# Optimization experiments

Measured on AMD Instinct MI355X. Metric: run time of the kernel, lower is better.

Reference implementation:

```python
import jax, jax.numpy as jnp
import numpy as np

DIM = 256; NH = 8; WH = 8; WW = 8; N = WH * WW
B, T, M, H, W = 2, 4, 5, 64, 64
HD = DIM // NH
SCALE = HD ** -0.5

def _rel_pos_index():
    coords = np.stack(np.meshgrid(np.arange(WH), np.arange(WW), indexing='ij'))
    cf = coords.reshape(2, -1)
    rc = (cf[:, :, None] - cf[:, None, :]).transpose(1, 2, 0)
    rc[:, :, 0] += WH - 1
    rc[:, :, 1] += WW - 1
    rc[:, :, 0] *= 2 * WW - 1
    return rc.sum(-1)  # (N, N) ints in [0, (2WH-1)(2WW-1))

RPI = _rel_pos_index()

def layer_norm(x, g, b, eps=1e-5):
    mu = x.mean(-1, keepdims=True)
    var = jnp.mean((x - mu) ** 2, axis=-1, keepdims=True)
    return (x - mu) * jax.lax.rsqrt(var + eps) * g + b

def setup_inputs():
    key = jax.random.key(0)
    ks = jax.random.split(key, 32)
    C = DIM
    w = lambda i, shape, s=0.02: jax.random.normal(ks[i], shape, jnp.float32) * s
    return {
        'x': jax.random.normal(ks[0], (B, T, H, W, C), jnp.float32),
        'kv': jax.random.normal(ks[1], (B, M, H, W, C), jnp.float32),
        'mask_matrix': jnp.zeros(((H // WH) * (W // WW), N, N), jnp.float32),
        'norm_q_g': jnp.ones((C,), jnp.float32), 'norm_q_b': jnp.zeros((C,), jnp.float32),
        'norm_kv_g': jnp.ones((C,), jnp.float32), 'norm_kv_b': jnp.zeros((C,), jnp.float32),
        'q_w': w(2, (C, C)), 'q_b': w(3, (C,)),
        'kv_w': w(4, (2 * C, C)), 'kv_b': w(5, (2 * C,)),
        'rpb_table': w(6, ((2 * WH - 1) * (2 * WW - 1), NH)),
        'pos_emb': jax.random.normal(ks[7], (N, C), jnp.float32) / C ** 0.5,
        'pq_w': w(8, (C, C)), 'pq_b': w(9, (C,)),
        'pk_w': w(10, (C, C)), 'pk_b': w(11, (C,)),
        'pv_w': w(12, (C, C)), 'pv_b': w(13, (C,)),
        'po_w': w(14, (C, C)), 'po_b': w(15, (C,)),
        'proj_w': w(16, (C, C)), 'proj_b': w(17, (C,)),
        'norm2_g': jnp.ones((C,), jnp.float32), 'norm2_b': jnp.zeros((C,), jnp.float32),
        'mlp_w1': w(18, (4 * C, C)), 'mlp_b1': w(19, (4 * C,)),
        'mlp_w2': w(20, (C, 4 * C)), 'mlp_b2': w(21, (C,)),
    }

def _attention_pool(xw, pos_emb, pq_w, pq_b, pk_w, pk_b, pv_w, pv_b, po_w, po_b):
    # CLIP-style attention pooling: xw (b, M, N, C) -> (b, N, C)
    b, m, n, C = xw.shape
    avg = xw.mean(axis=1, keepdims=True)
    xw = jnp.concatenate([avg, xw], axis=1) + pos_emb[None, None]  # (b, M+1, N, C)
    tok = xw.reshape(b, (m + 1) * n, C)  # flattened (m n) token axis
    q = (tok[:, :n] @ pq_w.T + pq_b).reshape(b, n, NH, HD).transpose(0, 2, 1, 3) * HD ** -0.5
    k = (tok @ pk_w.T + pk_b).reshape(b, -1, NH, HD).transpose(0, 2, 1, 3)
    v = (tok @ pv_w.T + pv_b).reshape(b, -1, NH, HD).transpose(0, 2, 1, 3)
    a = jax.nn.softmax(jnp.einsum('bhqd,bhkd->bhqk', q, k), axis=-1)
    o = jnp.einsum('bhqk,bhkd->bhqd', a, v).transpose(0, 2, 1, 3).reshape(b, n, C)
    return o @ po_w.T + po_b

def reference(x, kv, mask_matrix, norm_q_g, norm_q_b, norm_kv_g, norm_kv_b,
              q_w, q_b, kv_w, kv_b, rpb_table, pos_emb,
              pq_w, pq_b, pk_w, pk_b, pv_w, pv_b, po_w, po_b,
              proj_w, proj_b, norm2_g, norm2_b, mlp_w1, mlp_b1, mlp_w2, mlp_b2):
    Bv, Tv, Hv, Wv, C = x.shape
    Mv = kv.shape[1]
    nWh, nWw = Hv // WH, Wv // WW
    nW = nWh * nWw
    B_ = Bv * nW
    shortcut = x
    xq = layer_norm(x, norm_q_g, norm_q_b)
    xk = layer_norm(kv, norm_kv_g, norm_kv_b)

    def part(z, S):  # window partition (B,S,H,W,C) -> (B*nW, S, N, C)
        z = z.reshape(Bv, S, nWh, WH, nWw, WW, C)
        return z.transpose(0, 2, 4, 1, 3, 5, 6).reshape(B_, S, N, C)

    qw = part(xq, Tv)
    kvw = part(xk, Mv)
    q = (qw @ q_w.T + q_b).reshape(B_, Tv, N, NH, HD).transpose(0, 1, 3, 2, 4)   # (B_,T,h,N,d)
    kvp = (kvw @ kv_w.T + kv_b).reshape(B_, Mv, N, 2, NH, HD)
    k = kvp[:, :, :, 0].transpose(0, 1, 3, 2, 4)                                  # (B_,M,h,N,d)
    v = kvp[:, :, :, 1].transpose(0, 1, 3, 2, 4)
    attn = jnp.einsum('bthnd,bmhkd->btmhnk', q * SCALE, k)                        # (B_,T,M,h,N,N)
    rpb = rpb_table[RPI.reshape(-1)].reshape(N, N, NH).transpose(2, 0, 1)         # (h,N,N)
    attn = jax.nn.softmax(attn + rpb[None, None, None], axis=-1)  # shift=(0,0) -> mask_matrix unused
    out = jnp.einsum('btmhnk,bmhkd->btmhnd', attn, v)                             # (B_,T,M,h,N,d)
    # faithful to torch: transpose(1,2) (swap T/M) then flat reshape to (B_,T,M,N,C)
    out = out.transpose(0, 2, 1, 3, 4, 5).reshape(B_, Tv, Mv, N, C)
    out = out.reshape(B_ * Tv, Mv, N, C)
    out = _attention_pool(out, pos_emb, pq_w, pq_b, pk_w, pk_b, pv_w, pv_b, po_w, po_b)
    out = out.reshape(B_, Tv, N, C)
    out = jax.nn.gelu(out, approximate=False)
    out = out @ proj_w.T + proj_b
    # window reverse -> (B,T,H,W,C)
    out = out.reshape(Bv, nWh, nWw, Tv, WH, WW, C).transpose(0, 3, 1, 4, 2, 5, 6).reshape(Bv, Tv, Hv, Wv, C)
    x1 = shortcut + out
    h = layer_norm(x1, norm2_g, norm2_b)
    h = jax.nn.gelu(h @ mlp_w1.T + mlp_b1, approximate=False) @ mlp_w2.T + mlp_b2
    return x1 + h
```

## Files before the change

kernel.cpp:

```cpp
#include <hip/hip_runtime.h>
#include <hip/hip_bf16.h>
#include <cstddef>
#include <cstdint>

#define SCALE_QK 0.17677669529663687f

typedef __attribute__((ext_vector_type(8))) short bf16x8;
typedef __attribute__((ext_vector_type(4))) float f32x4;

__global__ __launch_bounds__(256) void convb_kernel(
    const float* __restrict__ src, __hip_bfloat16* __restrict__ dst, int n) {
  int i = blockIdx.x * 256 + threadIdx.x;
  if (i < n) dst[i] = __float2bfloat16(src[i]);
}

__global__ __launch_bounds__(256) void rpbx_kernel(
    const float* __restrict__ rpb_table, ushort* __restrict__ rpbx) {
  int gid = blockIdx.x * 256 + threadIdx.x;
  int h = gid >> 12;
  int rest = gid & 4095;
  int n = rest >> 6, j = rest & 63;
  int i1 = n >> 3, j1 = n & 7, i2 = j >> 3, j2 = j & 7;
  float v = rpb_table[((i1 - i2 + 7) * 15 + (j1 - j2 + 7)) * 8 + h];
  __hip_bfloat16 b = __float2bfloat16(v);
  rpbx[gid] = *reinterpret_cast<ushort*>(&b);
}

__global__ __launch_bounds__(256) void ln_part_kernel(
    const float* __restrict__ in, __hip_bfloat16* __restrict__ out,
    const float* __restrict__ gamma, const float* __restrict__ beta,
    int S, int b0) {
  int r = blockIdx.x;
  int n = r & 63;
  int tmp = r >> 6;
  int s = tmp % S;
  int b_ = b0 + tmp / S;
  int b  = b_ >> 6;
  int wh = (b_ >> 3) & 7;
  int ww = b_ & 7;
  int gh = wh * 8 + (n >> 3);
  int gw = ww * 8 + (n & 7);
  const float* src = in + (((size_t)(b * S + s) * 64 + gh) * 64 + gw) * 256;
  int c = threadIdx.x;
  float v = src[c];
  __shared__ float red[256];
  red[c] = v; __syncthreads();
  for (int off = 128; off > 0; off >>= 1) { if (c < off) red[c] += red[c + off]; __syncthreads(); }
  float mu = red[0] * (1.f / 256.f);
  __syncthreads();
  float dv = v - mu;
  red[c] = dv * dv; __syncthreads();
  for (int off = 128; off > 0; off >>= 1) { if (c < off) red[c] += red[c + off]; __syncthreads(); }
  float var = red[0] * (1.f / 256.f);
  out[(size_t)r * 256 + c] = __float2bfloat16(dv * rsqrtf(var + 1e-5f) * gamma[c] + beta[c]);
}

__global__ __launch_bounds__(256) void ln_plain_kernel(
    const float* __restrict__ in, __hip_bfloat16* __restrict__ out,
    const float* __restrict__ gamma, const float* __restrict__ beta) {
  int r = blockIdx.x;
  const float* src = in + (size_t)r * 256;
  int c = threadIdx.x;
  float v = src[c];
  __shared__ float red[256];
  red[c] = v; __syncthreads();
  for (int off = 128; off > 0; off >>= 1) { if (c < off) red[c] += red[c + off]; __syncthreads(); }
  float mu = red[0] * (1.f / 256.f);
  __syncthreads();
  float dv = v - mu;
  red[c] = dv * dv; __syncthreads();
  for (int off = 128; off > 0; off >>= 1) { if (c < off) red[c] += red[c + off]; __syncthreads(); }
  float var = red[0] * (1.f / 256.f);
  out[(size_t)r * 256 + c] = __float2bfloat16(dv * rsqrtf(var + 1e-5f) * gamma[c] + beta[c]);
}

__global__ __launch_bounds__(256) void mgemm_kernel(
    const ushort* __restrict__ A, const ushort* __restrict__ W,
    const float* __restrict__ bias, const float* __restrict__ resid,
    void* __restrict__ Cp, int Mrows, int N, int K, int flags) {
  __shared__ ushort As[128 * 64];
  __shared__ ushort Bs[128 * 64];
  int tid = threadIdx.x;
  int lane = tid & 63, wid = tid >> 6;
  int wm = wid >> 1, wn = wid & 1;
  int row0 = blockIdx.y * 128, col0 = blockIdx.x * 128;
  int srow = tid >> 3;
  int slot = tid & 7;
  f32x4 acc[4][4];
  #pragma unroll
  for (int m = 0; m < 4; ++m)
    #pragma unroll
    for (int n = 0; n < 4; ++n) acc[m][n] = (f32x4){0.f, 0.f, 0.f, 0.f};

  for (int k0 = 0; k0 < K; k0 += 64) {
    #pragma unroll
    for (int i = 0; i < 4; ++i) {
      int r = i * 32 + srow;
      int gr = row0 + r; if (gr >= Mrows) gr = Mrows - 1;
      bf16x8 va = *(const bf16x8*)(A + (size_t)gr * K + k0 + slot * 8);
      int gc = col0 + r;
      bf16x8 vb = *(const bf16x8*)(W + (size_t)gc * K + k0 + slot * 8);
      int ldso = r * 64 + ((slot ^ (r & 7)) << 3);
      *(bf16x8*)(As + ldso) = va;
      *(bf16x8*)(Bs + ldso) = vb;
    }
    __syncthreads();
    #pragma unroll
    for (int ks = 0; ks < 2; ++ks) {
      bf16x8 af[4], bfr[4];
      int sgrp = ks * 4 + (lane >> 4);
      #pragma unroll
      for (int m = 0; m < 4; ++m) {
        int r = wm * 64 + m * 16 + (lane & 15);
        af[m] = *(const bf16x8*)(As + r * 64 + ((sgrp ^ (r & 7)) << 3));
      }
      #pragma unroll
      for (int n = 0; n < 4; ++n) {
        int r = wn * 64 + n * 16 + (lane & 15);
        bfr[n] = *(const bf16x8*)(Bs + r * 64 + ((sgrp ^ (r & 7)) << 3));
      }
      #pragma unroll
      for (int m = 0; m < 4; ++m)
        #pragma unroll
        for (int n = 0; n < 4; ++n)
          acc[m][n] = __builtin_amdgcn_mfma_f32_16x16x32_bf16(af[m], bfr[n], acc[m][n], 0, 0, 0);
    }
    __syncthreads();
  }

  float* Cf = (float*)Cp;
  __hip_bfloat16* Cb = (__hip_bfloat16*)Cp;
  #pragma unroll
  for (int m = 0; m < 4; ++m) {
    #pragma unroll
    for (int n = 0; n < 4; ++n) {
      int col = col0 + wn * 64 + n * 16 + (lane & 15);
      #pragma unroll
      for (int r = 0; r < 4; ++r) {
        int row = row0 + wm * 64 + m * 16 + (lane >> 4) * 4 + r;
        if (row >= Mrows) continue;
        float v = acc[m][n][r] + (bias ? bias[col] : 0.f);
        if (flags & 1) v = 0.5f * v * (1.f + erff(v * 0.70710678118654752f));
        if (resid) v += resid[(size_t)row * N + col];
        if (flags & 2) Cb[(size_t)row * N + col] = __float2bfloat16(v);
        else           Cf[(size_t)row * N + col] = v;
      }
    }
  }
}

#define TBM 64
#define TBN 64
#define TBK 16
__global__ __launch_bounds__(256) void gemm_kernel(
    const float* __restrict__ A, const float* __restrict__ Wt,
    const float* __restrict__ bias, float* __restrict__ Cc,
    int Mrows, int Nout, int K) {
  __shared__ float Asl[TBK][TBM + 1];
  __shared__ float Wsl[TBK][TBN + 1];
  int tid = threadIdx.x;
  int tx = tid & 15, ty = tid >> 4;
  int row0 = blockIdx.y * TBM, col0 = blockIdx.x * TBN;
  float acc[4][4] = {};
  for (int k0 = 0; k0 < K; k0 += TBK) {
    #pragma unroll
    for (int t = 0; t < 4; ++t) {
      int idx = t * 256 + tid;
      int lm = idx >> 4, lk = idx & 15;
      int gr = row0 + lm;
      Asl[lk][lm] = (gr < Mrows) ? A[(size_t)gr * K + k0 + lk] : 0.f;
      int gc = col0 + lm;
      Wsl[lk][lm] = (gc < Nout) ? Wt[(size_t)gc * K + k0 + lk] : 0.f;
    }
    __syncthreads();
    #pragma unroll
    for (int kk = 0; kk < TBK; ++kk) {
      float a[4], b[4];
      #pragma unroll
      for (int i = 0; i < 4; ++i) a[i] = Asl[kk][ty * 4 + i];
      #pragma unroll
      for (int j = 0; j < 4; ++j) b[j] = Wsl[kk][tx * 4 + j];
      #pragma unroll
      for (int i = 0; i < 4; ++i)
        #pragma unroll
        for (int j = 0; j < 4; ++j)
          acc[i][j] = fmaf(a[i], b[j], acc[i][j]);
    }
    __syncthreads();
  }
  #pragma unroll
  for (int i = 0; i < 4; ++i) {
    int gr = row0 + ty * 4 + i;
    if (gr >= Mrows) continue;
    #pragma unroll
    for (int j = 0; j < 4; ++j) {
      int gc = col0 + tx * 4 + j;
      if (gc >= Nout) continue;
      Cc[(size_t)gr * Nout + gc] = acc[i][j] + bias[gc];
    }
  }
}

__global__ __launch_bounds__(256) void wattn_kernel(
    const float* __restrict__ qb, const float* __restrict__ kvp,
    const ushort* __restrict__ rpbx, __hip_bfloat16* __restrict__ xw) {
  int idx = blockIdx.x;
  int h = idx & 7; idx >>= 3;
  int m = idx % 5;
  int b_l = idx / 5;
  int tid = threadIdx.x;
  int n = tid & 63;
  int w = tid >> 6;

  __shared__ float4 ks4[64][9];
  __shared__ float4 vs4[64][9];
  __shared__ ushort rpbs[64][65];

  {
    int sr = tid >> 2, dg = tid & 3;
    const float* base = kvp + (((size_t)(b_l * 5 + m) * 64 + sr) * 512) + h * 32 + dg * 8;
    float4 k0 = *(const float4*)(base);
    float4 k1 = *(const float4*)(base + 4);
    float4 v0 = *(const float4*)(base + 256);
    float4 v1 = *(const float4*)(base + 260);
    ks4[sr][dg * 2]     = k0;
    ks4[sr][dg * 2 + 1] = k1;
    vs4[sr][dg * 2]     = v0;
    vs4[sr][dg * 2 + 1] = v1;
  }
  {
    const ushort* rsrc = rpbx + h * 4096;
    #pragma unroll
    for (int e = tid; e < 4096; e += 256) rpbs[e >> 6][e & 63] = rsrc[e];
  }

  float qr[32];
  {
    const float* qrow = qb + (((size_t)(b_l * 4 + w) * 64 + n) * 256) + h * 32;
    #pragma unroll
    for (int i = 0; i < 8; ++i) {
      float4 qv = *(const float4*)(qrow + i * 4);
      qr[i*4+0] = qv.x * SCALE_QK; qr[i*4+1] = qv.y * SCALE_QK;
      qr[i*4+2] = qv.z * SCALE_QK; qr[i*4+3] = qv.w * SCALE_QK;
    }
  }
  __syncthreads();

  float mx = -1e30f, l = 0.f;
  float acc[32];
  #pragma unroll
  for (int d = 0; d < 32; ++d) acc[d] = 0.f;

  #pragma unroll
  for (int st = 0; st < 4; ++st) {
    float s[16];
    float cmx = mx;
    #pragma unroll
    for (int jj = 0; jj < 16; ++jj) {
      int j = st * 16 + jj;
      float a0 = 0.f, a1 = 0.f;
      #pragma unroll
      for (int i = 0; i < 4; ++i) {
        float4 k0 = ks4[j][i * 2];
        float4 k1 = ks4[j][i * 2 + 1];
        a0 = fmaf(qr[i*8+0], k0.x, a0);
        a0 = fmaf(qr[i*8+1], k0.y, a0);
        a0 = fmaf(qr[i*8+2], k0.z, a0);
        a0 = fmaf(qr[i*8+3], k0.w, a0);
        a1 = fmaf(qr[i*8+4], k1.x, a1);
        a1 = fmaf(qr[i*8+5], k1.y, a1);
        a1 = fmaf(qr[i*8+6], k1.z, a1);
        a1 = fmaf(qr[i*8+7], k1.w, a1);
      }
      ushort rb = rpbs[n][j];
      float bias = __bfloat162float(*reinterpret_cast<__hip_bfloat16*>(&rb));
      float sb = a0 + a1 + bias;
      s[jj] = sb;
      cmx = fmaxf(cmx, sb);
    }
    float sc = __expf(mx - cmx);
    l *= sc;
    #pragma unroll
    for (int d = 0; d < 32; ++d) acc[d] *= sc;
    #pragma unroll
    for (int jj = 0; jj < 16; ++jj) {
      int j = st * 16 + jj;
      float p = __expf(s[jj] - cmx);
      l += p;
      #pragma unroll
      for (int i = 0; i < 8; ++i) {
        float4 vv = vs4[j][i];
        acc[i*4+0] = fmaf(p, vv.x, acc[i*4+0]);
        acc[i*4+1] = fmaf(p, vv.y, acc[i*4+1]);
        acc[i*4+2] = fmaf(p, vv.z, acc[i*4+2]);
        acc[i*4+3] = fmaf(p, vv.w, acc[i*4+3]);
      }
    }
    mx = cmx;
  }
  float inv = 1.f / l;

  int f = m * 4 + w;
  int tp = f / 5, mp = f % 5;
  int np = h * 8 + (n >> 3);
  int cp = (n & 7) * 32;
  size_t base = ((((size_t)(b_l * 4 + tp) * 5 + mp) * 64 + np) * 256) + cp;
  #pragma unroll
  for (int d = 0; d < 32; ++d) xw[base + d] = __float2bfloat16(acc[d] * inv);
}

__global__ __launch_bounds__(256) void avg3_kernel(
    const __hip_bfloat16* __restrict__ xw, const float* __restrict__ pk,
    const float* __restrict__ pv, const float* __restrict__ pos_emb,
    __hip_bfloat16* __restrict__ avgq, float* __restrict__ pka,
    float* __restrict__ pva) {
  int gid = blockIdx.x * 256 + threadIdx.x;
  int c = gid & 255;
  int rn = gid >> 8;
  int n = rn & 63;
  int bp = rn >> 6;
  size_t base = ((size_t)bp * 320 + n) * 256 + c;
  const size_t stride = 64 * 256;
  float sq = 0.f, sk = 0.f, sv = 0.f;
  #pragma unroll
  for (int m = 0; m < 5; ++m) {
    sq += __bfloat162float(xw[base + m * stride]);
    sk += pk[base + m * stride];
    sv += pv[base + m * stride];
  }
  avgq[(size_t)rn * 256 + c] = __float2bfloat16(sq * 0.2f + pos_emb[n * 256 + c]);
  pka[(size_t)rn * 256 + c] = sk * 0.2f;
  pva[(size_t)rn * 256 + c] = sv * 0.2f;
}

__global__ __launch_bounds__(256) void pattn_kernel(
    const float* __restrict__ pq, const float* __restrict__ pk,
    const float* __restrict__ pv, const float* __restrict__ pka,
    const float* __restrict__ pva, const float* __restrict__ pos_pk,
    const float* __restrict__ pos_pv, __hip_bfloat16* __restrict__ o) {
  int h = blockIdx.x & 7;
  int bp = blockIdx.x >> 3;
  int tid = threadIdx.x;
  int lane = tid & 63;
  int w = tid >> 6;
  __shared__ float4 ks4[64][9];
  __shared__ float4 vs4[64][9];
  __shared__ float sm[4][64];
  __shared__ float sl[4][64];
  __shared__ float sacc[4][64][32];

  int sr = tid >> 2, dg = tid & 3;
  const float* ppkp = pos_pk + sr * 256 + h * 32 + dg * 8;
  const float* ppvp = pos_pv + sr * 256 + h * 32 + dg * 8;
  float4 ppk0 = *(const float4*)(ppkp);
  float4 ppk1 = *(const float4*)(ppkp + 4);
  float4 ppv0 = *(const float4*)(ppvp);
  float4 ppv1 = *(const float4*)(ppvp + 4);

  float qr[32];
  {
    const float* qrow = pq + (((size_t)bp * 64 + lane) * 256) + h * 32;
    #pragma unroll
    for (int i = 0; i < 8; ++i) {
      float4 qv = *(const float4*)(qrow + i * 4);
      qr[i*4+0] = qv.x * SCALE_QK; qr[i*4+1] = qv.y * SCALE_QK;
      qr[i*4+2] = qv.z * SCALE_QK; qr[i*4+3] = qv.w * SCALE_QK;
    }
  }

  float mx = -1e30f, l = 0.f;
  float acc[32];
  #pragma unroll
  for (int d = 0; d < 32; ++d) acc[d] = 0.f;

  for (int mm = 0; mm < 6; ++mm) {
    const float* kr;
    const float* vr;
    if (mm == 0) {
      kr = pka + (((size_t)bp * 64 + sr) * 256) + h * 32 + dg * 8;
      vr = pva + (((size_t)bp * 64 + sr) * 256) + h * 32 + dg * 8;
    } else {
      kr = pk + (((size_t)(bp * 5 + mm - 1) * 64 + sr) * 256) + h * 32 + dg * 8;
      vr = pv + (((size_t)(bp * 5 + mm - 1) * 64 + sr) * 256) + h * 32 + dg * 8;
    }
    __syncthreads();
    {
      float4 a0 = *(const float4*)(kr);
      float4 a1 = *(const float4*)(kr + 4);
      float4 b0 = *(const float4*)(vr);
      float4 b1 = *(const float4*)(vr + 4);
      ks4[sr][dg*2]   = make_float4(a0.x+ppk0.x, a0.y+ppk0.y, a0.z+ppk0.z, a0.w+ppk0.w);
      ks4[sr][dg*2+1] = make_float4(a1.x+ppk1.x, a1.y+ppk1.y, a1.z+ppk1.z, a1.w+ppk1.w);
      vs4[sr][dg*2]   = make_float4(b0.x+ppv0.x, b0.y+ppv0.y, b0.z+ppv0.z, b0.w+ppv0.w);
      vs4[sr][dg*2+1] = make_float4(b1.x+ppv1.x, b1.y+ppv1.y, b1.z+ppv1.z, b1.w+ppv1.w);
    }
    __syncthreads();

    float s[16];
    float cmx = mx;
    #pragma unroll
    for (int jj = 0; jj < 16; ++jj) {
      int j = w * 16 + jj;
      float a = 0.f;
      #pragma unroll
      for (int i = 0; i < 8; ++i) {
        float4 kk = ks4[j][i];
        a = fmaf(qr[i*4+0], kk.x, a);
        a = fmaf(qr[i*4+1], kk.y, a);
        a = fmaf(qr[i*4+2], kk.z, a);
        a = fmaf(qr[i*4+3], kk.w, a);
      }
      s[jj] = a;
      cmx = fmaxf(cmx, a);
    }
    float scale = __expf(mx - cmx);
    l *= scale;
    #pragma unroll
    for (int d = 0; d < 32; ++d) acc[d] *= scale;
    #pragma unroll
    for (int jj = 0; jj < 16; ++jj) {
      int j = w * 16 + jj;
      float p = __expf(s[jj] - cmx);
      l += p;
      #pragma unroll
      for (int i = 0; i < 8; ++i) {
        float4 vv = vs4[j][i];
        acc[i*4+0] = fmaf(p, vv.x, acc[i*4+0]);
        acc[i*4+1] = fmaf(p, vv.y, acc[i*4+1]);
        acc[i*4+2] = fmaf(p, vv.z, acc[i*4+2]);
        acc[i*4+3] = fmaf(p, vv.w, acc[i*4+3]);
      }
    }
    mx = cmx;
  }

  sm[w][lane] = mx;
  sl[w][lane] = l;
  #pragma unroll
  for (int d = 0; d < 32; ++d) sacc[w][lane][d] = acc[d];
  __syncthreads();

  float M = fmaxf(fmaxf(sm[0][lane], sm[1][lane]), fmaxf(sm[2][lane], sm[3][lane]));
  float e0 = __expf(sm[0][lane] - M);
  float e1 = __expf(sm[1][lane] - M);
  float e2 = __expf(sm[2][lane] - M);
  float e3 = __expf(sm[3][lane] - M);
  float L = sl[0][lane]*e0 + sl[1][lane]*e1 + sl[2][lane]*e2 + sl[3][lane]*e3;
  float inv = 1.f / L;
  size_t base = (((size_t)bp * 64 + lane) * 256) + h * 32 + w * 8;
  #pragma unroll
  for (int dd = 0; dd < 8; ++dd) {
    int d = w * 8 + dd;
    float sv = sacc[0][lane][d]*e0 + sacc[1][lane][d]*e1
             + sacc[2][lane][d]*e2 + sacc[3][lane][d]*e3;
    o[base + dd] = __float2bfloat16(sv * inv);
  }
}

__global__ __launch_bounds__(256) void scatter_kernel(
    const float* __restrict__ x, const float* __restrict__ prj,
    float* __restrict__ out, int b0) {
  int gid = blockIdx.x * 256 + threadIdx.x;
  int c = gid & 255;
  int r = gid >> 8;
  int n = r & 63;
  int t = (r >> 6) & 3;
  int b_l = r >> 8;
  int b_ = b0 + b_l;
  int b = b_ >> 6, wh = (b_ >> 3) & 7, ww = b_ & 7;
  int gh = wh * 8 + (n >> 3), gw = ww * 8 + (n & 7);
  size_t pix = (((size_t)(b * 4 + t) * 64 + gh) * 64 + gw) * 256 + c;
  out[pix] = x[pix] + prj[(size_t)r * 256 + c];
}

extern "C" void kernel_launch(void* const* d_in, const int* in_sizes, int n_in,
                              void* d_out, int out_size, void* d_ws, size_t ws_size,
                              hipStream_t stream) {
  const float* x       = (const float*)d_in[0];
  const float* kv      = (const float*)d_in[1];
  const float* nq_g    = (const float*)d_in[3];
  const float* nq_b    = (const float*)d_in[4];
  const float* nk_g    = (const float*)d_in[5];
  const float* nk_b    = (const float*)d_in[6];
  const float* q_w     = (const float*)d_in[7];
  const float* q_b     = (const float*)d_in[8];
  const float* kv_w    = (const float*)d_in[9];
  const float* kv_b    = (const float*)d_in[10];
  const float* rpb     = (const float*)d_in[11];
  const float* pos_emb = (const float*)d_in[12];
  const float* pq_w    = (const float*)d_in[13];
  const float* pq_b    = (const float*)d_in[14];
  const float* pk_w    = (const float*)d_in[15];
  const float* pk_b    = (const float*)d_in[16];
  const float* pv_w    = (const float*)d_in[17];
  const float* pv_b    = (const float*)d_in[18];
  const float* po_w    = (const float*)d_in[19];
  const float* po_b    = (const float*)d_in[20];
  const float* proj_w  = (const float*)d_in[21];
  const float* proj_b  = (const float*)d_in[22];
  const float* n2_g    = (const float*)d_in[23];
  const float* n2_b    = (const float*)d_in[24];
  const float* mlp_w1  = (const float*)d_in[25];
  const float* mlp_b1  = (const float*)d_in[26];
  const float* mlp_w2  = (const float*)d_in[27];
  const float* mlp_b2  = (const float*)d_in[28];
  float* out = (float*)d_out;
  float* ws = (float*)d_ws;

  size_t wsF = ws_size / sizeof(float);
  float* pospk = ws;
  float* pospv = ws + 16384;
  __hip_bfloat16* wq_b    = (__hip_bfloat16*)(ws + 32768);
  __hip_bfloat16* wkv_b   = (__hip_bfloat16*)(ws + 65536);
  __hip_bfloat16* wpq_b   = (__hip_bfloat16*)(ws + 131072);
  __hip_bfloat16* wpk_b   = (__hip_bfloat16*)(ws + 163840);
  __hip_bfloat16* wpv_b   = (__hip_bfloat16*)(ws + 196608);
  __hip_bfloat16* wpo_b   = (__hip_bfloat16*)(ws + 229376);
  __hip_bfloat16* wproj_b = (__hip_bfloat16*)(ws + 262144);
  __hip_bfloat16* wm1_b   = (__hip_bfloat16*)(ws + 294912);
  __hip_bfloat16* wm2_b   = (__hip_bfloat16*)(ws + 425984);
  ushort* rpbx            = (ushort*)(ws + 557056);
  const size_t FIXED = 573440;

  int CH = 0;
  const int cands[7] = {64, 32, 16, 8, 4, 2, 1};
  for (int i = 0; i < 7; ++i) {
    size_t need = FIXED + (size_t)1179648 * cands[i];
    if (need <= wsF) { CH = cands[i]; break; }
  }
  if (CH == 0) return;
  size_t CHs = (size_t)CH;
  float* cb = ws + FIXED;

  __hip_bfloat16* qw_b  = (__hip_bfloat16*)cb;
  __hip_bfloat16* kvw_b = (__hip_bfloat16*)(cb + 32768 * CHs);
  float* qb2 = cb + 73728 * CHs;
  float* kvp = cb + 139264 * CHs;
  float* PK  = cb;
  float* PV  = cb + 327680 * CHs;
  __hip_bfloat16* xw_b  = (__hip_bfloat16*)(cb + 655360 * CHs);
  __hip_bfloat16* AVG_b = (__hip_bfloat16*)(cb + 819200 * CHs);
  float* PQ  = cb + 851968 * CHs;
  float* PKA = cb + 917504 * CHs;
  float* PVA = cb + 983040 * CHs;
  __hip_bfloat16* OC_b = (__hip_bfloat16*)(cb + 1048576 * CHs);
  __hip_bfloat16* PG_b = (__hip_bfloat16*)(cb + 1081344 * CHs);
  float* PRJ = cb + 1114112 * CHs;

  gemm_kernel<<<dim3(4, 1), 256, 0, stream>>>(pos_emb, pk_w, pk_b, pospk, 64, 256, 256);
  gemm_kernel<<<dim3(4, 1), 256, 0, stream>>>(pos_emb, pv_w, pv_b, pospv, 64, 256, 256);
  rpbx_kernel<<<128, 256, 0, stream>>>(rpb, rpbx);
  convb_kernel<<<256,  256, 0, stream>>>(q_w,    wq_b,    65536);
  convb_kernel<<<512,  256, 0, stream>>>(kv_w,   wkv_b,   131072);
  convb_kernel<<<256,  256, 0, stream>>>(pq_w,   wpq_b,   65536);
  convb_kernel<<<256,  256, 0, stream>>>(pk_w,   wpk_b,   65536);
  convb_kernel<<<256,  256, 0, stream>>>(pv_w,   wpv_b,   65536);
  convb_kernel<<<256,  256, 0, stream>>>(po_w,   wpo_b,   65536);
  convb_kernel<<<256,  256, 0, stream>>>(proj_w, wproj_b, 65536);
  convb_kernel<<<1024, 256, 0, stream>>>(mlp_w1, wm1_b,   262144);
  convb_kernel<<<1024, 256, 0, stream>>>(mlp_w2, wm2_b,   262144);

  for (int c0 = 0; c0 < 128; c0 += CH) {
    int rowsQ  = CH * 256;
    int rowsKV = CH * 320;
    int rowsXW = CH * 1280;
    int bpC    = CH * 4;
    int rowsP  = bpC * 64;
    ln_part_kernel<<<rowsQ, 256, 0, stream>>>(x, qw_b, nq_g, nq_b, 4, c0);
    ln_part_kernel<<<rowsKV, 256, 0, stream>>>(kv, kvw_b, nk_g, nk_b, 5, c0);
    mgemm_kernel<<<dim3(2, rowsQ / 128), 256, 0, stream>>>(
        (const ushort*)qw_b, (const ushort*)wq_b, q_b, nullptr, qb2, rowsQ, 256, 256, 0);
    mgemm_kernel<<<dim3(4, (rowsKV + 127) / 128), 256, 0, stream>>>(
        (const ushort*)kvw_b, (const ushort*)wkv_b, kv_b, nullptr, kvp, rowsKV, 512, 256, 0);
    wattn_kernel<<<CH * 40, 256, 0, stream>>>(qb2, kvp, rpbx, xw_b);
    mgemm_kernel<<<dim3(2, rowsXW / 128), 256, 0, stream>>>(
        (const ushort*)xw_b, (const ushort*)wpk_b, nullptr, nullptr, PK, rowsXW, 256, 256, 0);
    mgemm_kernel<<<dim3(2, rowsXW / 128), 256, 0, stream>>>(
        (const ushort*)xw_b, (const ushort*)wpv_b, nullptr, nullptr, PV, rowsXW, 256, 256, 0);
    avg3_kernel<<<rowsP, 256, 0, stream>>>(xw_b, PK, PV, pos_emb, AVG_b, PKA, PVA);
    mgemm_kernel<<<dim3(2, rowsP / 128), 256, 0, stream>>>(
        (const ushort*)AVG_b, (const ushort*)wpq_b, pq_b, nullptr, PQ, rowsP, 256, 256, 0);
    pattn_kernel<<<bpC * 8, 256, 0, stream>>>(PQ, PK, PV, PKA, PVA, pospk, pospv, OC_b);
    mgemm_kernel<<<dim3(2, rowsP / 128), 256, 0, stream>>>(
        (const ushort*)OC_b, (const ushort*)wpo_b, po_b, nullptr, PG_b, rowsP, 256, 256, 3);
    mgemm_kernel<<<dim3(2, rowsP / 128), 256, 0, stream>>>(
        (const ushort*)PG_b, (const ushort*)wproj_b, proj_b, nullptr, PRJ, rowsP, 256, 256, 0);
    scatter_kernel<<<rowsP, 256, 0, stream>>>(x, PRJ, out, c0);
  }

  int R = 32768;
  while ((size_t)R * 640 > (size_t)1179648 * CHs && R > 128) R >>= 1;
  __hip_bfloat16* ln2c = (__hip_bfloat16*)cb;
  __hip_bfloat16* h1c  = (__hip_bfloat16*)(cb + 128 * (size_t)R);
  for (int r0 = 0; r0 < 32768; r0 += R) {
    ln_plain_kernel<<<R, 256, 0, stream>>>(out + (size_t)r0 * 256, ln2c, n2_g, n2_b);
    mgemm_kernel<<<dim3(8, R / 128), 256, 0, stream>>>(
        (const ushort*)ln2c, (const ushort*)wm1_b, mlp_b1, nullptr, h1c, R, 1024, 256, 3);
    mgemm_kernel<<<dim3(2, R / 128), 256, 0, stream>>>(
        (const ushort*)h1c, (const ushort*)wm2_b, mlp_b2, out + (size_t)r0 * 256,
        out + (size_t)r0 * 256, R, 256, 1024, 0);
  }
}
```

Baseline: 1.846 ms.

## Split pooling attention keys across 8 lanes per query with shuffle merge

The pooling attention kernel now runs 512 threads per block, with each query handled by 8 lanes that each process an interleaved subset of keys. The per-lane softmax partials are merged with xor shuffles instead of a shared-memory cross-wave reduction, and the large sacc shared buffer is removed. The goal is more parallelism per block and less shared memory and synchronization. In exchange, each merge step shuffles all 32 accumulator registers, and the wider blocks may hurt occupancy.

```diff
diff --git a/kernel.cpp b/kernel.cpp
--- a/kernel.cpp
+++ b/kernel.cpp
@@ -333,7 +333,7 @@
   pva[(size_t)rn * 256 + c] = sv * 0.2f;
 }
 
-__global__ __launch_bounds__(256) void pattn_kernel(
+__global__ __launch_bounds__(512) void pattn_kernel(
     const float* __restrict__ pq, const float* __restrict__ pk,
     const float* __restrict__ pv, const float* __restrict__ pka,
     const float* __restrict__ pva, const float* __restrict__ pos_pk,
@@ -343,23 +343,21 @@
   int tid = threadIdx.x;
   int lane = tid & 63;
   int w = tid >> 6;
+  int q = w * 8 + (lane >> 3);
+  int kg = lane & 7;
+
   __shared__ float4 ks4[64][9];
   __shared__ float4 vs4[64][9];
-  __shared__ float sm[4][64];
-  __shared__ float sl[4][64];
-  __shared__ float sacc[4][64][32];
-
-  int sr = tid >> 2, dg = tid & 3;
-  const float* ppkp = pos_pk + sr * 256 + h * 32 + dg * 8;
-  const float* ppvp = pos_pv + sr * 256 + h * 32 + dg * 8;
-  float4 ppk0 = *(const float4*)(ppkp);
-  float4 ppk1 = *(const float4*)(ppkp + 4);
-  float4 ppv0 = *(const float4*)(ppvp);
-  float4 ppv1 = *(const float4*)(ppvp + 4);
+
+  int sr = tid >> 3, dg = tid & 7;
+  const float* ppkp = pos_pk + sr * 256 + h * 32 + dg * 4;
+  const float* ppvp = pos_pv + sr * 256 + h * 32 + dg * 4;
+  float4 ppk = *(const float4*)(ppkp);
+  float4 ppv = *(const float4*)(ppvp);
 
   float qr[32];
   {
-    const float* qrow = pq + (((size_t)bp * 64 + lane) * 256) + h * 32;
+    const float* qrow = pq + (((size_t)bp * 64 + q) * 256) + h * 32;
     #pragma unroll
     for (int i = 0; i < 8; ++i) {
       float4 qv = *(const float4*)(qrow + i * 4);
@@ -377,50 +375,52 @@
     const float* kr;
     const float* vr;
     if (mm == 0) {
-      kr = pka + (((size_t)bp * 64 + sr) * 256) + h * 32 + dg * 8;
-      vr = pva + (((size_t)bp * 64 + sr) * 256) + h * 32 + dg * 8;
+      kr = pka + (((size_t)bp * 64 + sr) * 256) + h * 32 + dg * 4;
+      vr = pva + (((size_t)bp * 64 + sr) * 256) + h * 32 + dg * 4;
     } else {
-      kr = pk + (((size_t)(bp * 5 + mm - 1) * 64 + sr) * 256) + h * 32 + dg * 8;
-      vr = pv + (((size_t)(bp * 5 + mm - 1) * 64 + sr) * 256) + h * 32 + dg * 8;
+      kr = pk + (((size_t)(bp * 5 + mm - 1) * 64 + sr) * 256) + h * 32 + dg * 4;
+      vr = pv + (((size_t)(bp * 5 + mm - 1) * 64 + sr) * 256) + h * 32 + dg * 4;
     }
     __syncthreads();
     {
-      float4 a0 = *(const float4*)(kr);
-      float4 a1 = *(const float4*)(kr + 4);
-      float4 b0 = *(const float4*)(vr);
-      float4 b1 = *(const float4*)(vr + 4);
-      ks4[sr][dg*2]   = make_float4(a0.x+ppk0.x, a0.y+ppk0.y, a0.z+ppk0.z, a0.w+ppk0.w);
-      ks4[sr][dg*2+1] = make_float4(a1.x+ppk1.x, a1.y+ppk1.y, a1.z+ppk1.z, a1.w+ppk1.w);
-      vs4[sr][dg*2]   = make_float4(b0.x+ppv0.x, b0.y+ppv0.y, b0.z+ppv0.z, b0.w+ppv0.w);
-      vs4[sr][dg*2+1] = make_float4(b1.x+ppv1.x, b1.y+ppv1.y, b1.z+ppv1.z, b1.w+ppv1.w);
+      float4 a = *(const float4*)(kr);
+      float4 b = *(const float4*)(vr);
+      ks4[sr][dg] = make_float4(a.x + ppk.x, a.y + ppk.y, a.z + ppk.z, a.w + ppk.w);
+      vs4[sr][dg] = make_float4(b.x + ppv.x, b.y + ppv.y, b.z + ppv.z, b.w + ppv.w);
     }
     __syncthreads();
 
-    float s[16];
+    float s8[8];
     float cmx = mx;
     #pragma unroll
-    for (int jj = 0; jj < 16; ++jj) {
-      int j = w * 16 + jj;
-      float a = 0.f;
-      #pragma unroll
-      for (int i = 0; i < 8; ++i) {
-        float4 kk = ks4[j][i];
-        a = fmaf(qr[i*4+0], kk.x, a);
-        a = fmaf(qr[i*4+1], kk.y, a);
-        a = fmaf(qr[i*4+2], kk.z, a);
-        a = fmaf(qr[i*4+3], kk.w, a);
+    for (int ss = 0; ss < 8; ++ss) {
+      int j = ss * 8 + kg;
+      float a0 = 0.f, a1 = 0.f;
+      #pragma unroll
+      for (int i = 0; i < 4; ++i) {
+        float4 k0 = ks4[j][i * 2];
+        float4 k1 = ks4[j][i * 2 + 1];
+        a0 = fmaf(qr[i*8+0], k0.x, a0);
+        a0 = fmaf(qr[i*8+1], k0.y, a0);
+        a0 = fmaf(qr[i*8+2], k0.z, a0);
+        a0 = fmaf(qr[i*8+3], k0.w, a0);
+        a1 = fmaf(qr[i*8+4], k1.x, a1);
+        a1 = fmaf(qr[i*8+5], k1.y, a1);
+        a1 = fmaf(qr[i*8+6], k1.z, a1);
+        a1 = fmaf(qr[i*8+7], k1.w, a1);
       }
-      s[jj] = a;
-      cmx = fmaxf(cmx, a);
-    }
-    float scale = __expf(mx - cmx);
-    l *= scale;
-    #pragma unroll
-    for (int d = 0; d < 32; ++d) acc[d] *= scale;
-    #pragma unroll
-    for (int jj = 0; jj < 16; ++jj) {
-      int j = w * 16 + jj;
-      float p = __expf(s[jj] - cmx);
+      float sb = a0 + a1;
+      s8[ss] = sb;
+      cmx = fmaxf(cmx, sb);
+    }
+    float sc = __expf(mx - cmx);
+    l *= sc;
+    #pragma unroll
+    for (int d = 0; d < 32; ++d) acc[d] *= sc;
+    #pragma unroll
+    for (int ss = 0; ss < 8; ++ss) {
+      int j = ss * 8 + kg;
+      float p = __expf(s8[ss] - cmx);
       l += p;
       #pragma unroll
       for (int i = 0; i < 8; ++i) {
@@ -434,27 +434,27 @@
     mx = cmx;
   }
 
-  sm[w][lane] = mx;
-  sl[w][lane] = l;
-  #pragma unroll
-  for (int d = 0; d < 32; ++d) sacc[w][lane][d] = acc[d];
-  __syncthreads();
-
-  float M = fmaxf(fmaxf(sm[0][lane], sm[1][lane]), fmaxf(sm[2][lane], sm[3][lane]));
-  float e0 = __expf(sm[0][lane] - M);
-  float e1 = __expf(sm[1][lane] - M);
-  float e2 = __expf(sm[2][lane] - M);
-  float e3 = __expf(sm[3][lane] - M);
-  float L = sl[0][lane]*e0 + sl[1][lane]*e1 + sl[2][lane]*e2 + sl[3][lane]*e3;
-  float inv = 1.f / L;
-  size_t base = (((size_t)bp * 64 + lane) * 256) + h * 32 + w * 8;
-  #pragma unroll
-  for (int dd = 0; dd < 8; ++dd) {
-    int d = w * 8 + dd;
-    float sv = sacc[0][lane][d]*e0 + sacc[1][lane][d]*e1
-             + sacc[2][lane][d]*e2 + sacc[3][lane][d]*e3;
-    o[base + dd] = __float2bfloat16(sv * inv);
-  }
+  #pragma unroll
+  for (int mask = 1; mask < 8; mask <<= 1) {
+    float mo = __shfl_xor(mx, mask);
+    float lo = __shfl_xor(l, mask);
+    float M = fmaxf(mx, mo);
+    float es = __expf(mx - M);
+    float eo = __expf(mo - M);
+    l = l * es + lo * eo;
+    #pragma unroll
+    for (int d = 0; d < 32; ++d) {
+      float ao = __shfl_xor(acc[d], mask);
+      acc[d] = acc[d] * es + ao * eo;
+    }
+    mx = M;
+  }
+  float inv = 1.f / l;
+
+  size_t base = (((size_t)bp * 64 + q) * 256) + h * 32 + kg * 4;
+  #pragma unroll
+  for (int dd = 0; dd < 4; ++dd)
+    o[base + dd] = __float2bfloat16(acc[kg * 4 + dd] * inv);
 }
 
 __global__ __launch_bounds__(256) void scatter_kernel(
@@ -580,7 +580,7 @@
     avg3_kernel<<<rowsP, 256, 0, stream>>>(xw_b, PK, PV, pos_emb, AVG_b, PKA, PVA);
     mgemm_kernel<<<dim3(2, rowsP / 128), 256, 0, stream>>>(
         (const ushort*)AVG_b, (const ushort*)wpq_b, pq_b, nullptr, PQ, rowsP, 256, 256, 0);
-    pattn_kernel<<<bpC * 8, 256, 0, stream>>>(PQ, PK, PV, PKA, PVA, pospk, pospv, OC_b);
+    pattn_kernel<<<bpC * 8, 512, 0, stream>>>(PQ, PK, PV, PKA, PVA, pospk, pospv, OC_b);
     mgemm_kernel<<<dim3(2, rowsP / 128), 256, 0, stream>>>(
         (const ushort*)OC_b, (const ushort*)wpo_b, po_b, nullptr, PG_b, rowsP, 256, 256, 3);
     mgemm_kernel<<<dim3(2, rowsP / 128), 256, 0, stream>>>(
```

Measured after the change: 1.747 ms. 5.4% less time.
